# Kernel optimization log

Measured on AMD Instinct MI355X. Metric: run time of the kernel, lower is better.

The kernel has to match this reference:

```python
import jax, jax.numpy as jnp
import numpy as np

B, NIN, L, N, K, NOUT = 4096, 512, 16, 512, 32, 256
TOTAL = NIN + L * N  # 8704 total nodes in the DAG


def setup_inputs() -> dict:
    key = jax.random.key(0)
    ks = jax.random.split(key, 5)
    x = jax.random.normal(ks[0], (B, NIN), jnp.float32)
    W = jax.random.normal(ks[1], (L, N, K), jnp.float32) * 0.2
    b = jax.random.normal(ks[2], (L, N), jnp.float32) * 0.1
    W_out = jax.random.normal(ks[3], (NOUT, K), jnp.float32) * 0.2
    b_out = jax.random.normal(ks[4], (NOUT,), jnp.float32) * 0.1
    rng = np.random.default_rng(0)
    # layer l may only read nodes computed before it (topological validity)
    idx = np.stack([rng.integers(0, NIN + l * N, size=(N, K)) for l in range(L)]).astype(np.int32)
    idx_out = rng.integers(0, TOTAL, size=(NOUT, K)).astype(np.int32)
    return {"x": x, "W": W, "b": b, "W_out": W_out, "b_out": b_out,
            "idx": jnp.asarray(idx), "idx_out": jnp.asarray(idx_out)}


def reference(x, W, b, W_out, b_out, idx, idx_out):
    # buffer of all node activations, filled topologically (out_dict analog)
    buf0 = jnp.zeros((B, TOTAL), x.dtype).at[:, :NIN].set(x)

    def step(carry, layer):
        buf, l = carry
        li, lW, lb = layer
        gathered = buf[:, li]  # [B, N, K] irregular gather of predecessor outputs
        out = jax.nn.sigmoid(jnp.einsum('bnk,nk->bn', gathered, lW) + lb)  # per-node tiny linear + sigmoid
        buf = jax.lax.dynamic_update_slice(buf, out, (0, NIN + l * N))
        return (buf, l + 1), None

    (buf, _), _ = jax.lax.scan(step, (buf0, jnp.int32(0)), (idx, W, b))
    g = buf[:, idx_out]  # [B, NOUT, K]
    return jax.nn.sigmoid(jnp.einsum('bok,ok->bo', g, W_out) + b_out)
```

## Files before the change

### kernel.cpp

```cpp
#include <hip/hip_runtime.h>
#include <hip/hip_fp16.h>
#include <math.h>

#define B     4096
#define NIN   512
#define L     16
#define N     512
#define K     32
#define NOUT  256
#define HID   (L * N)
#define TOTAL (NIN + L * N)
#define BROWS 16
#define BLOCK 512
#define XBASE (TOTAL * 16)
#define LDS_BYTES (XBASE + NIN * 32)

typedef __attribute__((ext_vector_type(4))) unsigned int u32x4;
typedef __attribute__((ext_vector_type(8))) _Float16 h8;

#define XSCL (255.0f / 11.0f)
#define XOFF 5.5f

__device__ __forceinline__ float sigmoidf_fast(float z) {
    return 1.0f / (1.0f + __expf(-z));
}

__global__ __launch_bounds__(64)
void repack_kernel(const float* __restrict__ W,
                   const int*   __restrict__ idx,
                   const float* __restrict__ W_out,
                   const int*   __restrict__ idx_out,
                   const float* __restrict__ b,
                   const float* __restrict__ b_out,
                   unsigned* __restrict__ packed,
                   float*    __restrict__ biasw)
{
    const int n = blockIdx.x * 64 + threadIdx.x;
    const int* ip; const float* wp; float bb;
    if (n < HID) {
        ip = idx + (size_t)n * K;  wp = W + (size_t)n * K;  bb = b[n];
    } else {
        const int m = n - HID;
        ip = idx_out + (size_t)m * K;  wp = W_out + (size_t)m * K;  bb = b_out[m];
    }
    const bool l0 = (n < N);
    unsigned* po = packed + (size_t)n * K;

#pragma unroll
    for (int q = 0; q < 8; ++q) {
        const int4   a = ((const int4*)ip)[q];
        const float4 f = ((const float4*)wp)[q];
        const int   cc[4] = {a.x, a.y, a.z, a.w};
        const float ww[4] = {f.x, f.y, f.z, f.w};
#pragma unroll
        for (int kq = 0; kq < 4; ++kq) {
            const int c = cc[kq]; const float w = ww[kq];
            float wprime;
            if (l0)            { wprime = w; }
            else if (c < NIN)  { wprime = w * (11.0f / 255.0f); bb -= XOFF * w; }
            else               { wprime = w * (1.0f / 255.0f); }
            const unsigned short h =
                __builtin_bit_cast(unsigned short, (_Float16)wprime);
            po[q * 4 + kq] = ((unsigned)c << 16) | h;
        }
    }
    biasw[n] = bb;
}

#define GATH8(PW, Q0, D)                                                      \
    _Pragma("unroll")                                                         \
    for (int jj = 0; jj < 8; ++jj) {                                          \
        const unsigned u = (PW)[((Q0) + jj) >> 2][((Q0) + jj) & 3];           \
        const int ad = (int)((u >> 16) << 4);                                 \
        (D)[jj] = *(const u32x4*)(lds + ad);                                  \
    }

#define FMAU8(PW, Q0, D, FA)                                                  \
    _Pragma("unroll")                                                         \
    for (int jj = 0; jj < 8; ++jj) {                                          \
        const unsigned u = (PW)[((Q0) + jj) >> 2][((Q0) + jj) & 3];           \
        const float wf = (float)__builtin_bit_cast(                           \
            _Float16, (unsigned short)(u & 0xFFFFu));                         \
        const u32x4 dd = (D)[jj];                                             \
        _Pragma("unroll")                                                     \
        for (int w2 = 0; w2 < 4; ++w2)                                        \
            _Pragma("unroll")                                                 \
            for (int r = 0; r < 4; ++r)                                       \
                (FA)[w2 * 4 + r] = fmaf(                                      \
                    (float)((dd[w2] >> (8 * r)) & 0xFFu), wf,                 \
                    (FA)[w2 * 4 + r]);                                        \
    }

#define EPI(FA, BB, ENT)                                                      \
    {                                                                         \
        u32x4 ow;                                                             \
        _Pragma("unroll")                                                     \
        for (int i2 = 0; i2 < 4; ++i2) {                                      \
            unsigned dw = 0;                                                  \
            _Pragma("unroll")                                                 \
            for (int j2 = 0; j2 < 4; ++j2) {                                  \
                const float sg = sigmoidf_fast((FA)[4 * i2 + j2] + (BB));     \
                dw |= ((unsigned)fmaf(sg, 255.f, 0.5f)) << (8 * j2);          \
            }                                                                 \
            ow[i2] = dw;                                                      \
        }                                                                     \
        *(u32x4*)(lds + (size_t)(ENT) * 16) = ow;                             \
    }

#define LAYERU8(PW, BB, ENT)                                                  \
    {                                                                         \
        u32x4 d0[8], d1[8], d2[8], d3[8];                                     \
        float fa[16];                                                         \
        _Pragma("unroll") for (int i0 = 0; i0 < 16; ++i0) fa[i0] = 0.f;       \
        GATH8(PW, 0, d0) GATH8(PW, 8, d1) GATH8(PW, 16, d2)                   \
        FMAU8(PW, 0, d0, fa)                                                  \
        GATH8(PW, 24, d3)                                                     \
        FMAU8(PW, 8, d1, fa) FMAU8(PW, 16, d2, fa) FMAU8(PW, 24, d3, fa)      \
        EPI(fa, BB, ENT)                                                      \
    }

#define LAYER0(PW, BB, ENT)                                                   \
    {                                                                         \
        float fa[16];                                                         \
        _Pragma("unroll") for (int i0 = 0; i0 < 16; ++i0) fa[i0] = 0.f;       \
        _Pragma("unroll")                                                     \
        for (int j = 0; j < 32; ++j) {                                        \
            const unsigned u = (PW)[j >> 2][j & 3];                           \
            const int ad = XBASE + (int)((u >> 16) << 5);                     \
            const h8 lo = *(const h8*)(lds + ad);                             \
            const h8 hi = *(const h8*)(lds + ad + 16);                        \
            const float wf = (float)__builtin_bit_cast(                       \
                _Float16, (unsigned short)(u & 0xFFFFu));                     \
            _Pragma("unroll")                                                 \
            for (int r = 0; r < 8; ++r) {                                     \
                fa[r]     = fmaf((float)lo[r], wf, fa[r]);                    \
                fa[8 + r] = fmaf((float)hi[r], wf, fa[8 + r]);                \
            }                                                                 \
        }                                                                     \
        EPI(fa, BB, ENT)                                                      \
    }

__global__ __launch_bounds__(BLOCK, 2)
void ffnet_kernel(const float* __restrict__ x,
                  const unsigned* __restrict__ packed,
                  const float*    __restrict__ biasw,
                  float* __restrict__ out)
{
    extern __shared__ char lds[];

    const int t  = threadIdx.x;
    const int r0 = blockIdx.x * BROWS;

    {
        float xv[16];
#pragma unroll
        for (int r = 0; r < 16; ++r) xv[r] = x[(size_t)(r0 + r) * NIN + t];
        h8 hx0, hx1;
#pragma unroll
        for (int r = 0; r < 8; ++r) {
            hx0[r] = (_Float16)xv[r];
            hx1[r] = (_Float16)xv[8 + r];
        }
        *(h8*)(lds + XBASE + t * 32)      = hx0;
        *(h8*)(lds + XBASE + t * 32 + 16) = hx1;
        u32x4 ux;
#pragma unroll
        for (int i = 0; i < 4; ++i) {
            unsigned dw = 0;
#pragma unroll
            for (int j2 = 0; j2 < 4; ++j2) {
                const float q = fminf(
                    fmaxf(fmaf(xv[4 * i + j2] + XOFF, XSCL, 0.5f), 0.f), 255.f);
                dw |= ((unsigned)q) << (8 * j2);
            }
            ux[i] = dw;
        }
        *(u32x4*)(lds + t * 16) = ux;
    }

    u32x4 pa[8], pb[8];
    float ba, bb;
    {
        const u32x4* pp = (const u32x4*)(packed + (size_t)t * K);
#pragma unroll
        for (int q = 0; q < 8; ++q) pa[q] = pp[q];
        ba = biasw[t];
    }
    __syncthreads();

    {
        const u32x4* pp = (const u32x4*)(packed + (size_t)(N + t) * K);
#pragma unroll
        for (int q = 0; q < 8; ++q) pb[q] = pp[q];
        bb = biasw[N + t];
    }
    LAYER0(pa, ba, (NIN + t))
    __syncthreads();

    for (int l = 1; l < 15; l += 2) {
        {
            const u32x4* pp = (const u32x4*)(packed + (size_t)((l + 1) * N + t) * K);
#pragma unroll
            for (int q = 0; q < 8; ++q) pa[q] = pp[q];
            ba = biasw[(l + 1) * N + t];
        }
        LAYERU8(pb, bb, (NIN + l * N + t))
        __syncthreads();
        {
            const u32x4* pp = (const u32x4*)(packed + (size_t)((l + 2) * N + t) * K);
#pragma unroll
            for (int q = 0; q < 8; ++q) pb[q] = pp[q];
            bb = biasw[(l + 2) * N + t];
        }
        LAYERU8(pa, ba, (NIN + (l + 1) * N + t))
        __syncthreads();
    }

    if (t < NOUT) {
        const u32x4* pp = (const u32x4*)(packed + (size_t)(HID + t) * K);
#pragma unroll
        for (int q = 0; q < 8; ++q) pa[q] = pp[q];
        ba = biasw[HID + t];
    }
    LAYERU8(pb, bb, (NIN + 15 * N + t))
    __syncthreads();

    if (t < NOUT) {
        u32x4 d0[8], d1[8], d2[8], d3[8];
        float fa[16];
#pragma unroll
        for (int i0 = 0; i0 < 16; ++i0) fa[i0] = 0.f;
        GATH8(pa, 0, d0) GATH8(pa, 8, d1) GATH8(pa, 16, d2)
        FMAU8(pa, 0, d0, fa)
        GATH8(pa, 24, d3)
        FMAU8(pa, 8, d1, fa) FMAU8(pa, 16, d2, fa) FMAU8(pa, 24, d3, fa)

#pragma unroll
        for (int r = 0; r < 16; ++r)
            out[(size_t)(r0 + r) * NOUT + t] = sigmoidf_fast(fa[r] + ba);
    }
}

extern "C" void kernel_launch(void* const* d_in, const int* in_sizes, int n_in,
                              void* d_out, int out_size, void* d_ws, size_t ws_size,
                              hipStream_t stream) {
    const float* x     = (const float*)d_in[0];
    const float* W     = (const float*)d_in[1];
    const float* b     = (const float*)d_in[2];
    const float* W_out = (const float*)d_in[3];
    const float* b_out = (const float*)d_in[4];
    const int*   idx   = (const int*)d_in[5];
    const int*   idx_o = (const int*)d_in[6];
    float* out = (float*)d_out;

    char* ws = (char*)d_ws;
    unsigned* packed = (unsigned*)(ws);
    float*    biasw  = (float*)   (ws + 1081344);

    repack_kernel<<<dim3((HID + NOUT) / 64), dim3(64), 0, stream>>>(
        W, idx, W_out, idx_o, b, b_out, packed, biasw);

    ffnet_kernel<<<dim3(B / BROWS), dim3(BLOCK), LDS_BYTES, stream>>>(
        x, packed, biasw, out);
}
```

Before: 166.3 us.

## Use packed fp16 dot2 with magic-number byte-to-half conversion in inner loops

Replaces the per-byte unpack, convert and fmaf inner loop with v_perm byte packing into fp16 using the 0x6400 magic exponent trick, then v_dot2_f32_f16 over pairs of predecessors. The constant offset of 1024 that the trick adds is folded into the bias during repacking. Layer 0 is likewise rewritten to pair fp16 inputs via perm and dot2. This roughly halves the VALU instruction count per accumulation but changes rounding slightly, because activations are now multiplied against fp16 weights inside dot2 with the bias correction applied in fp32.

Measured after the change: 157.0 us. 1.06x faster.

```diff
diff --git a/kernel.cpp b/kernel.cpp
--- a/kernel.cpp
+++ b/kernel.cpp
@@ -15,6 +15,7 @@
 #define XBASE (TOTAL * 16)
 #define LDS_BYTES (XBASE + NIN * 32)
 
+typedef __attribute__((ext_vector_type(2))) _Float16 hv2;
 typedef __attribute__((ext_vector_type(4))) unsigned int u32x4;
 typedef __attribute__((ext_vector_type(8))) _Float16 h8;
 
@@ -23,6 +24,14 @@
 
 __device__ __forceinline__ float sigmoidf_fast(float z) {
     return 1.0f / (1.0f + __expf(-z));
+}
+
+__device__ __forceinline__ float fdot2f(hv2 a, hv2 b, float c) {
+#if defined(__has_builtin) && __has_builtin(__builtin_amdgcn_fdot2)
+    return __builtin_amdgcn_fdot2(a, b, c, false);
+#else
+    return fmaf((float)a.x, (float)b.x, fmaf((float)a.y, (float)b.y, c));
+#endif
 }
 
 __global__ __launch_bounds__(64)
@@ -57,11 +66,15 @@
             const int c = cc[kq]; const float w = ww[kq];
             float wprime;
             if (l0)            { wprime = w; }
-            else if (c < NIN)  { wprime = w * (11.0f / 255.0f); bb -= XOFF * w; }
+            else if (c < NIN)  { wprime = w * (11.0f / 255.0f); }
             else               { wprime = w * (1.0f / 255.0f); }
-            const unsigned short h =
-                __builtin_bit_cast(unsigned short, (_Float16)wprime);
-            po[q * 4 + kq] = ((unsigned)c << 16) | h;
+            const _Float16 wh_ = (_Float16)wprime;
+            if (!l0) {
+                bb -= 1024.0f * (float)wh_;
+                if (c < NIN) bb -= XOFF * w;
+            }
+            po[q * 4 + kq] =
+                ((unsigned)c << 16) | __builtin_bit_cast(unsigned short, wh_);
         }
     }
     biasw[n] = bb;
@@ -75,20 +88,31 @@
         (D)[jj] = *(const u32x4*)(lds + ad);                                  \
     }
 
-#define FMAU8(PW, Q0, D, FA)                                                  \
+#define FDOT_PAIR(UJ, UJ1, DJ, DJ1, FA)                                       \
+    {                                                                         \
+        const hv2 w2_ = __builtin_bit_cast(hv2,                               \
+            __builtin_amdgcn_perm((UJ1), (UJ), 0x05040100u));                 \
+        _Pragma("unroll")                                                     \
+        for (int d_ = 0; d_ < 4; ++d_) {                                      \
+            _Pragma("unroll")                                                 \
+            for (int r_ = 0; r_ < 4; ++r_) {                                  \
+                const unsigned pb_ = __builtin_amdgcn_perm(                   \
+                    (DJ1)[d_], (DJ)[d_],                                      \
+                    0x0C000C00u | ((unsigned)(4 + r_) << 16) | (unsigned)r_)  \
+                    | 0x64006400u;                                            \
+                (FA)[4 * d_ + r_] = fdot2f(                                   \
+                    __builtin_bit_cast(hv2, pb_), w2_, (FA)[4 * d_ + r_]);    \
+            }                                                                 \
+        }                                                                     \
+    }
+
+#define FDOT_BATCH(PW, Q0, D, FA)                                             \
     _Pragma("unroll")                                                         \
-    for (int jj = 0; jj < 8; ++jj) {                                          \
-        const unsigned u = (PW)[((Q0) + jj) >> 2][((Q0) + jj) & 3];           \
-        const float wf = (float)__builtin_bit_cast(                           \
-            _Float16, (unsigned short)(u & 0xFFFFu));                         \
-        const u32x4 dd = (D)[jj];                                             \
-        _Pragma("unroll")                                                     \
-        for (int w2 = 0; w2 < 4; ++w2)                                        \
-            _Pragma("unroll")                                                 \
-            for (int r = 0; r < 4; ++r)                                       \
-                (FA)[w2 * 4 + r] = fmaf(                                      \
-                    (float)((dd[w2] >> (8 * r)) & 0xFFu), wf,                 \
-                    (FA)[w2 * 4 + r]);                                        \
+    for (int m_ = 0; m_ < 4; ++m_) {                                          \
+        const unsigned uj_  = (PW)[((Q0) + 2 * m_) >> 2][((Q0) + 2 * m_) & 3];\
+        const unsigned uj1_ =                                                 \
+            (PW)[((Q0) + 2 * m_ + 1) >> 2][((Q0) + 2 * m_ + 1) & 3];          \
+        FDOT_PAIR(uj_, uj1_, (D)[2 * m_], (D)[2 * m_ + 1], FA)                \
     }
 
 #define EPI(FA, BB, ENT)                                                      \
@@ -107,16 +131,46 @@
         *(u32x4*)(lds + (size_t)(ENT) * 16) = ow;                             \
     }
 
+#define LAYERU8BODY(PW, FA)                                                   \
+    u32x4 d0[8], d1[8], d2[8], d3[8];                                         \
+    _Pragma("unroll") for (int i0 = 0; i0 < 16; ++i0) (FA)[i0] = 0.f;         \
+    GATH8(PW, 0, d0) GATH8(PW, 8, d1) GATH8(PW, 16, d2)                       \
+    FDOT_BATCH(PW, 0, d0, FA)                                                 \
+    GATH8(PW, 24, d3)                                                         \
+    FDOT_BATCH(PW, 8, d1, FA)                                                 \
+    FDOT_BATCH(PW, 16, d2, FA)                                                \
+    FDOT_BATCH(PW, 24, d3, FA)
+
 #define LAYERU8(PW, BB, ENT)                                                  \
     {                                                                         \
-        u32x4 d0[8], d1[8], d2[8], d3[8];                                     \
         float fa[16];                                                         \
-        _Pragma("unroll") for (int i0 = 0; i0 < 16; ++i0) fa[i0] = 0.f;       \
-        GATH8(PW, 0, d0) GATH8(PW, 8, d1) GATH8(PW, 16, d2)                   \
-        FMAU8(PW, 0, d0, fa)                                                  \
-        GATH8(PW, 24, d3)                                                     \
-        FMAU8(PW, 8, d1, fa) FMAU8(PW, 16, d2, fa) FMAU8(PW, 24, d3, fa)      \
+        LAYERU8BODY(PW, fa)                                                   \
         EPI(fa, BB, ENT)                                                      \
+    }
+
+#define L0PAIR(UJ, UJ1, LWJ, LWJ1, HWJ, HWJ1, FA)                             \
+    {                                                                         \
+        const hv2 w2_ = __builtin_bit_cast(hv2,                               \
+            __builtin_amdgcn_perm((UJ1), (UJ), 0x05040100u));                 \
+        _Pragma("unroll")                                                     \
+        for (int p_ = 0; p_ < 4; ++p_) {                                      \
+            const unsigned pe_ = __builtin_amdgcn_perm(                       \
+                (LWJ1)[p_], (LWJ)[p_], 0x05040100u);                          \
+            const unsigned po_ = __builtin_amdgcn_perm(                       \
+                (LWJ1)[p_], (LWJ)[p_], 0x07060302u);                          \
+            (FA)[2 * p_]     = fdot2f(__builtin_bit_cast(hv2, pe_), w2_,      \
+                                      (FA)[2 * p_]);                          \
+            (FA)[2 * p_ + 1] = fdot2f(__builtin_bit_cast(hv2, po_), w2_,      \
+                                      (FA)[2 * p_ + 1]);                      \
+            const unsigned qe_ = __builtin_amdgcn_perm(                       \
+                (HWJ1)[p_], (HWJ)[p_], 0x05040100u);                          \
+            const unsigned qo_ = __builtin_amdgcn_perm(                       \
+                (HWJ1)[p_], (HWJ)[p_], 0x07060302u);                          \
+            (FA)[8 + 2 * p_]     = fdot2f(__builtin_bit_cast(hv2, qe_), w2_,  \
+                                          (FA)[8 + 2 * p_]);                  \
+            (FA)[8 + 2 * p_ + 1] = fdot2f(__builtin_bit_cast(hv2, qo_), w2_,  \
+                                          (FA)[8 + 2 * p_ + 1]);              \
+        }                                                                     \
     }
 
 #define LAYER0(PW, BB, ENT)                                                   \
@@ -124,17 +178,23 @@
         float fa[16];                                                         \
         _Pragma("unroll") for (int i0 = 0; i0 < 16; ++i0) fa[i0] = 0.f;       \
         _Pragma("unroll")                                                     \
-        for (int j = 0; j < 32; ++j) {                                        \
-            const unsigned u = (PW)[j >> 2][j & 3];                           \
-            const int ad = XBASE + (int)((u >> 16) << 5);                     \
-            const h8 lo = *(const h8*)(lds + ad);                             \
-            const h8 hi = *(const h8*)(lds + ad + 16);                        \
-            const float wf = (float)__builtin_bit_cast(                       \
-                _Float16, (unsigned short)(u & 0xFFFFu));                     \
+        for (int g = 0; g < 4; ++g) {                                         \
+            u32x4 lw[8], hw[8];                                               \
             _Pragma("unroll")                                                 \
-            for (int r = 0; r < 8; ++r) {                                     \
-                fa[r]     = fmaf((float)lo[r], wf, fa[r]);                    \
-                fa[8 + r] = fmaf((float)hi[r], wf, fa[8 + r]);                \
+            for (int j = 0; j < 8; ++j) {                                     \
+                const unsigned u = (PW)[(g * 8 + j) >> 2][(g * 8 + j) & 3];   \
+                const int ad = XBASE + (int)((u >> 16) << 5);                 \
+                lw[j] = *(const u32x4*)(lds + ad);                            \
+                hw[j] = *(const u32x4*)(lds + ad + 16);                       \
+            }                                                                 \
+            _Pragma("unroll")                                                 \
+            for (int m = 0; m < 4; ++m) {                                     \
+                const unsigned uj =                                           \
+                    (PW)[(g * 8 + 2 * m) >> 2][(g * 8 + 2 * m) & 3];          \
+                const unsigned uj1 =                                          \
+                    (PW)[(g * 8 + 2 * m + 1) >> 2][(g * 8 + 2 * m + 1) & 3];  \
+                L0PAIR(uj, uj1, lw[2 * m], lw[2 * m + 1],                     \
+                       hw[2 * m], hw[2 * m + 1], fa)                          \
             }                                                                 \
         }                                                                     \
         EPI(fa, BB, ENT)                                                      \
@@ -226,15 +286,8 @@
     __syncthreads();
 
     if (t < NOUT) {
-        u32x4 d0[8], d1[8], d2[8], d3[8];
         float fa[16];
-#pragma unroll
-        for (int i0 = 0; i0 < 16; ++i0) fa[i0] = 0.f;
-        GATH8(pa, 0, d0) GATH8(pa, 8, d1) GATH8(pa, 16, d2)
-        FMAU8(pa, 0, d0, fa)
-        GATH8(pa, 24, d3)
-        FMAU8(pa, 8, d1, fa) FMAU8(pa, 16, d2, fa) FMAU8(pa, 24, d3, fa)
-
+        LAYERU8BODY(pa, fa)
 #pragma unroll
         for (int r = 0; r < 16; ++r)
             out[(size_t)(r0 + r) * NOUT + t] = sigmoidf_fast(fa[r] + ba);
```
